# Kernel tuning notes

Hardware: AMD Instinct MI355X
Metric: run time of the kernel (lower is better)

The kernel has to match this reference:

```python
import jax, jax.numpy as jnp
import numpy as np

B, N, D, H, DK = 4, 2048, 1024, 16, 64  # batch, seq, model_dim, heads, key_dim (= value_dim)
NEG = -1e9


def setup_inputs() -> dict:
    key = jax.random.key(0)
    ks = jax.random.split(key, 5)
    X = jax.random.normal(ks[0], (B, N, D), dtype=jnp.float32)
    # causal additive mask [N, N]; module slices mask[:N, :M] and adds to logits
    mask = jnp.where(jnp.tril(jnp.ones((N, N), dtype=bool)), 0.0, NEG).astype(jnp.float32)
    s = 1.0 / np.sqrt(D)
    Wq = jax.random.normal(ks[1], (D, H * DK), dtype=jnp.float32) * s
    Wk = jax.random.normal(ks[2], (D, H * DK), dtype=jnp.float32) * s
    Wv = jax.random.normal(ks[3], (D, H * DK), dtype=jnp.float32) * s
    Wo = jax.random.normal(ks[4], (H * DK, D), dtype=jnp.float32) * s
    return {"X": X, "mask": mask, "Wq": Wq, "Wk": Wk, "Wv": Wv, "Wo": Wo}


def reference(X, mask, Wq, Wk, Wv, Wo):
    # Linear projections (bias=False), then split heads: [B,N,H,DK] -> [B,H,N,DK]
    Q = (X @ Wq).reshape(B, N, H, DK).transpose(0, 2, 1, 3)
    K = (X @ Wk).reshape(B, N, H, DK).transpose(0, 2, 1, 3)
    V = (X @ Wv).reshape(B, N, H, DK).transpose(0, 2, 1, 3)
    # full [B,H,N,N] attention logits (module materializes it explicitly)
    att = jnp.einsum('bhnd,bhmd->bhnm', Q, K) / jnp.sqrt(jnp.float32(DK))
    # dropout is in eval mode here -> identity; then additive mask[:N,:M]
    att = att + mask[:N, :N]
    prob = jax.nn.softmax(att, axis=-1)
    values = jnp.einsum('bhnm,bhmd->bhnd', prob, V)
    values_cat = values.transpose(0, 2, 1, 3).reshape(B, N, H * DK)
    return values_cat @ Wo
```

## Files before the change

### kernel.cpp

```cpp
#include <hip/hip_runtime.h>

typedef __fp16   f2  __attribute__((ext_vector_type(2)));
typedef _Float16 h4  __attribute__((ext_vector_type(4)));
typedef _Float16 v8h __attribute__((ext_vector_type(8)));
typedef float    v4f __attribute__((ext_vector_type(4)));
struct f2x2 { f2 lo, hi; };

#if __has_builtin(__builtin_amdgcn_exp2f)
#define FEXP2(x) __builtin_amdgcn_exp2f(x)
#else
#define FEXP2(x) exp2f(x)
#endif

constexpr int Bn = 4, Nn = 2048, Dn = 1024, Hn = 16, DKn = 64, Mn = 8192;

__device__ __forceinline__ void load_lds16(const _Float16* g, _Float16* l) {
    __builtin_amdgcn_global_load_lds(
        (const __attribute__((address_space(1))) void*)g,
        (__attribute__((address_space(3))) void*)l, 16, 0, 0);
}

__global__ __launch_bounds__(256) void cast_f16(const float* __restrict__ x,
                                                _Float16* __restrict__ y) {
    const int i = blockIdx.x * 256 + threadIdx.x;
    const float4 v = ((const float4*)x)[i];
    h4 o; o[0] = (_Float16)v.x; o[1] = (_Float16)v.y;
    o[2] = (_Float16)v.z; o[3] = (_Float16)v.w;
    ((h4*)y)[i] = o;
}

__global__ __launch_bounds__(256) void castW4(const float* __restrict__ Wq,
                                              const float* __restrict__ Wk,
                                              const float* __restrict__ Wv,
                                              const float* __restrict__ Wo,
                                              _Float16* __restrict__ Wqkv,
                                              _Float16* __restrict__ Wto) {
    __shared__ float tile[32][33];
    const int which = blockIdx.x >> 10, bid = blockIdx.x & 1023;
    const float* W = which == 0 ? Wq : which == 1 ? Wk : which == 2 ? Wv : Wo;
    _Float16* Dst = which < 3 ? (Wqkv + ((size_t)which << 20)) : Wto;
    const int bx = bid & 31, by = bid >> 5;
    const int t = threadIdx.x;
    const int r = t >> 3, c4 = (t & 7) * 4;
    const float4 v = *(const float4*)&W[(size_t)(by * 32 + r) * Dn + bx * 32 + c4];
    tile[r][c4 + 0] = v.x; tile[r][c4 + 1] = v.y;
    tile[r][c4 + 2] = v.z; tile[r][c4 + 3] = v.w;
    __syncthreads();
    h4 o;
    o[0] = (_Float16)tile[c4 + 0][r];
    o[1] = (_Float16)tile[c4 + 1][r];
    o[2] = (_Float16)tile[c4 + 2][r];
    o[3] = (_Float16)tile[c4 + 3][r];
    *(h4*)&Dst[(size_t)(bx * 32 + r) * Dn + by * 32 + c4] = o;
}

#define GEMM_KLOOP64(Abase, Bbase)                                                  \
    v4f acc[4][4];                                                                  \
    _Pragma("unroll") for (int i = 0; i < 4; ++i)                                   \
        _Pragma("unroll") for (int j = 0; j < 4; ++j) acc[i][j] = v4f{0,0,0,0};     \
    for (int k0 = 0; k0 < Dn; k0 += 64) {                                           \
        __syncthreads();                                                            \
        _Pragma("unroll") for (int jj = 0; jj < 4; ++jj) {                          \
            const int ci = jj * 256 + w * 64 + lane;                                \
            const int rs = ci >> 3, cs = ci & 7;                                    \
            const int gc = (cs ^ (rs & 7)) * 8;                                     \
            load_lds16(Abase + (size_t)rs * Dn + k0 + gc, &As[(jj*256 + w*64) * 8]);\
            load_lds16(Bbase + (size_t)rs * Dn + k0 + gc, &Bs[(jj*256 + w*64) * 8]);\
        }                                                                           \
        __syncthreads();                                                            \
        _Pragma("unroll") for (int ks2 = 0; ks2 < 2; ++ks2) {                       \
            v8h a[4], b[4];                                                         \
            _Pragma("unroll") for (int i = 0; i < 4; ++i) {                         \
                const int ar = wm*64 + i*16 + l16;                                  \
                a[i] = *(const v8h*)&As[ar * 64 + (((ks2*4 + quad) ^ (ar & 7)) * 8)];\
            }                                                                       \
            _Pragma("unroll") for (int j = 0; j < 4; ++j) {                         \
                const int br = wn*64 + j*16 + l16;                                  \
                b[j] = *(const v8h*)&Bs[br * 64 + (((ks2*4 + quad) ^ (br & 7)) * 8)];\
            }                                                                       \
            _Pragma("unroll") for (int i = 0; i < 4; ++i)                           \
                _Pragma("unroll") for (int j = 0; j < 4; ++j)                       \
                    acc[i][j] = __builtin_amdgcn_mfma_f32_16x16x32_f16(a[i], b[j],  \
                                                                   acc[i][j],0,0,0);\
        }                                                                           \
    }

__global__ __launch_bounds__(256) void gemmqkv(const _Float16* __restrict__ A,
                                               const _Float16* __restrict__ Wt,
                                               _Float16* __restrict__ Qo,
                                               _Float16* __restrict__ Ko,
                                               _Float16* __restrict__ Vo)
{
    __shared__ __align__(16) _Float16 As[128 * 64];
    __shared__ __align__(16) _Float16 Bs[128 * 64];
    const int t = threadIdx.x, lane = t & 63, w = t >> 6;
    const int quad = lane >> 4, l16 = lane & 15;
    const int wm = w >> 1, wn = w & 1;
    const int bx = blockIdx.x % 24, by = blockIdx.x / 24;
    const int m0 = by * 128, n0 = bx * 128;
    const _Float16* Abase = A + (size_t)m0 * Dn;
    const _Float16* Bbase = Wt + (size_t)n0 * Dn;

    GEMM_KLOOP64(Abase, Bbase)

    const int sec = n0 >> 10;
    if (sec < 2) {
        _Float16* C = sec ? Ko : Qo;
        const float scale = sec ? 1.0f : 0.125f * 1.44269504f;
#pragma unroll
        for (int i = 0; i < 4; ++i) {
            const int mbase = m0 + wm * 64 + i * 16 + quad * 4;
#pragma unroll
            for (int j = 0; j < 4; ++j) {
                const int nl = (n0 + wn * 64 + j * 16 + l16) & 1023;
                const int h = nl >> 6, dk = nl & 63;
#pragma unroll
                for (int r = 0; r < 4; ++r) {
                    const int m = mbase + r, b = m >> 11, nr = m & (Nn - 1);
                    C[((size_t)(b * Hn + h) * Nn + nr) * DKn + dk] = (_Float16)(acc[i][j][r] * scale);
                }
            }
        }
    } else {
#pragma unroll
        for (int i = 0; i < 4; ++i) {
            const int mbase = m0 + wm * 64 + i * 16 + quad * 4;
            const int b = mbase >> 11, nr = mbase & (Nn - 1);
#pragma unroll
            for (int j = 0; j < 4; ++j) {
                const int nl = (n0 + wn * 64 + j * 16 + l16) & 1023;
                const int h = nl >> 6, dk = nl & 63;
                h4 o; o[0] = (_Float16)acc[i][j][0]; o[1] = (_Float16)acc[i][j][1];
                o[2] = (_Float16)acc[i][j][2]; o[3] = (_Float16)acc[i][j][3];
                *(h4*)&Vo[((size_t)(b * Hn + h) * DKn + dk) * Nn + nr] = o;
            }
        }
    }
}

__global__ __launch_bounds__(256) void gemmo(const _Float16* __restrict__ A,
                                             const _Float16* __restrict__ Wt,
                                             float* __restrict__ C)
{
    __shared__ __align__(16) _Float16 As[128 * 64];
    __shared__ __align__(16) _Float16 Bs[128 * 64];
    const int t = threadIdx.x, lane = t & 63, w = t >> 6;
    const int quad = lane >> 4, l16 = lane & 15;
    const int wm = w >> 1, wn = w & 1;
    const int bx = blockIdx.x & 7, by = blockIdx.x >> 3;
    const int m0 = by * 128, n0 = bx * 128;
    const _Float16* Abase = A + (size_t)m0 * Dn;
    const _Float16* Bbase = Wt + (size_t)n0 * Dn;

    GEMM_KLOOP64(Abase, Bbase)

#pragma unroll
    for (int i = 0; i < 4; ++i) {
        const int mbase = m0 + wm * 64 + i * 16 + quad * 4;
#pragma unroll
        for (int j = 0; j < 4; ++j) {
            const int n = n0 + wn * 64 + j * 16 + l16;
#pragma unroll
            for (int r = 0; r < 4; ++r)
                C[(size_t)(mbase + r) * Dn + n] = acc[i][j][r];
        }
    }
}

__global__ __launch_bounds__(256) void flashv5(const _Float16* __restrict__ Q,
                                               const _Float16* __restrict__ K,
                                               const _Float16* __restrict__ Vt,
                                               _Float16* __restrict__ O)
{
    __shared__ __align__(16) _Float16 KS[64 * 64];
    __shared__ __align__(16) _Float16 VS[64 * 64];
    __shared__ __align__(16) _Float16 Ps[4][32 * 64];

    const int t = threadIdx.x;
    const int lane = t & 63, w = t >> 6;
    const int quad = lane >> 4, l16 = lane & 15;
    const int bh = blockIdx.x & 63;
    const int qtile = 15 - (blockIdx.x >> 6);
    const int b = bh >> 4, h = bh & 15;
    const int qb = qtile * 128 + w * 32;

    const _Float16* Qg = Q  + (size_t)bh * Nn * DKn;
    const _Float16* Kg = K  + (size_t)bh * Nn * DKn;
    const _Float16* Vg = Vt + (size_t)bh * DKn * Nn;

    auto stage = [&](int kt) {
        const int k0 = kt * 64;
#pragma unroll
        for (int jj = 0; jj < 2; ++jj) {
            const int ci = jj * 256 + w * 64 + lane;
            const int r = ci >> 3, c = ci & 7;
            const int gc = (c ^ (r & 7)) * 8;
            load_lds16(Kg + (size_t)(k0 + r) * DKn + gc, &KS[(jj * 256 + w * 64) * 8]);
            load_lds16(Vg + (size_t)r * Nn + k0 + gc,    &VS[(jj * 256 + w * 64) * 8]);
        }
    };
#define SWZ(arr, r, c) (*(const v8h*)&(arr)[(r) * 64 + (((c) ^ ((r) & 7)) * 8)])

    v8h qf[2][2];
#pragma unroll
    for (int qq = 0; qq < 2; ++qq)
#pragma unroll
        for (int ks = 0; ks < 2; ++ks)
            qf[qq][ks] = *(const v8h*)&Qg[(size_t)(qb + qq * 16 + l16) * DKn + ks * 32 + quad * 8];

    v8h ones;
#pragma unroll
    for (int i = 0; i < 8; ++i) ones[i] = (_Float16)1.0f;

    v4f o[2][4];
#pragma unroll
    for (int mq = 0; mq < 2; ++mq)
#pragma unroll
        for (int nt = 0; nt < 4; ++nt) o[mq][nt] = v4f{0.f, 0.f, 0.f, 0.f};
    v4f ol[2] = {v4f{0.f, 0.f, 0.f, 0.f}, v4f{0.f, 0.f, 0.f, 0.f}};

    const int NKT  = 2 * qtile + 2;
    const int diag = 2 * qtile + (w >> 1);

    for (int kt = 0; kt < NKT; ++kt) {
        stage(kt);
        __syncthreads();
        if (kt <= diag) {
            const int k0 = kt * 64;
            auto ptile = [&](bool domask) {
#pragma unroll
                for (int kk = 0; kk < 4; ++kk) {
                    v4f s0 = v4f{0.f, 0.f, 0.f, 0.f}, s1 = v4f{0.f, 0.f, 0.f, 0.f};
#pragma unroll
                    for (int ks = 0; ks < 2; ++ks) {
                        const v8h ak = SWZ(KS, kk * 16 + l16, ks * 4 + quad);
                        s0 = __builtin_amdgcn_mfma_f32_16x16x32_f16(ak, qf[0][ks], s0, 0, 0, 0);
                        s1 = __builtin_amdgcn_mfma_f32_16x16x32_f16(ak, qf[1][ks], s1, 0, 0, 0);
                    }
                    const int key0 = k0 + kk * 16 + quad * 4;
#pragma unroll
                    for (int qq = 0; qq < 2; ++qq) {
                        const v4f sv = qq ? s1 : s0;
                        const int q = qb + qq * 16 + l16;
                        float p[4];
#pragma unroll
                        for (int r = 0; r < 4; ++r) {
                            float x = sv[r];
                            if (domask) x = (key0 + r > q) ? -1e9f : x;
                            p[r] = FEXP2(x);
                        }
                        f2x2 pkr;
                        pkr.lo = __builtin_amdgcn_cvt_pkrtz(p[0], p[1]);
                        pkr.hi = __builtin_amdgcn_cvt_pkrtz(p[2], p[3]);
                        const h4 pk = __builtin_bit_cast(h4, pkr);
                        const int prow = qq * 16 + l16;
                        const int pch  = kk * 2 + (quad >> 1);
                        *(h4*)&Ps[w][prow * 64 + ((pch ^ (prow & 7)) * 8 + (quad & 1) * 4)] = pk;
                    }
                }
#pragma unroll
                for (int ks = 0; ks < 2; ++ks)
#pragma unroll
                    for (int mq = 0; mq < 2; ++mq) {
                        const int arow = mq * 16 + l16;
                        const int ach  = ks * 4 + quad;
                        const v8h a = *(const v8h*)&Ps[w][arow * 64 + ((ach ^ (arow & 7)) * 8)];
#pragma unroll
                        for (int nt = 0; nt < 4; ++nt) {
                            const v8h bvv = SWZ(VS, nt * 16 + l16, ks * 4 + quad);
                            o[mq][nt] = __builtin_amdgcn_mfma_f32_16x16x32_f16(a, bvv, o[mq][nt], 0, 0, 0);
                        }
                        ol[mq] = __builtin_amdgcn_mfma_f32_16x16x32_f16(a, ones, ol[mq], 0, 0, 0);
                    }
            };
            if (kt == diag) ptile(true); else ptile(false);
        }
        __syncthreads();
    }
#undef SWZ

    _Float16* Op = O + (size_t)b * Nn * Dn + h * DKn;
#pragma unroll
    for (int mq = 0; mq < 2; ++mq)
#pragma unroll
        for (int r = 0; r < 4; ++r) {
            const float li = 1.0f / ol[mq][r];
            const int qrow = qb + mq * 16 + quad * 4 + r;
#pragma unroll
            for (int nt = 0; nt < 4; ++nt)
                Op[(size_t)qrow * Dn + nt * 16 + l16] = (_Float16)(o[mq][nt][r] * li);
        }
}

extern "C" void kernel_launch(void* const* d_in, const int* in_sizes, int n_in,
                              void* d_out, int out_size, void* d_ws, size_t ws_size,
                              hipStream_t stream)
{
    const float* X  = (const float*)d_in[0];
    const float* Wq = (const float*)d_in[2];
    const float* Wk = (const float*)d_in[3];
    const float* Wv = (const float*)d_in[4];
    const float* Wo = (const float*)d_in[5];

    char* ws = (char*)d_ws;
    _Float16* Xh   = (_Float16*)ws;
    _Float16* Wqkv = (_Float16*)(ws + (16u << 20));
    _Float16* Wto  = Wqkv + (3u << 20);
    _Float16* Qh   = Wto + (1u << 20);
    _Float16* Kh   = Qh + (size_t)Mn * Dn;
    _Float16* Vth  = Kh + (size_t)Mn * Dn;
    _Float16* Ah   = Vth + (size_t)Mn * Dn;

    cast_f16<<<(Mn * Dn / 4) / 256, 256, 0, stream>>>(X, Xh);
    castW4<<<4096, 256, 0, stream>>>(Wq, Wk, Wv, Wo, Wqkv, Wto);
    gemmqkv<<<64 * 24, 256, 0, stream>>>(Xh, Wqkv, Qh, Kh, Vth);
    flashv5<<<1024, 256, 0, stream>>>(Qh, Kh, Vth, Ah);
    gemmo<<<512, 256, 0, stream>>>(Ah, Wto, (float*)d_out);
}
```

Measured before the change: 263.8 us.

## Pipeline projection GEMMs with multi-buffered LDS and larger 256x128 tiles

```diff
diff --git a/kernel.cpp b/kernel.cpp
--- a/kernel.cpp
+++ b/kernel.cpp
@@ -54,115 +54,146 @@
     *(h4*)&Dst[(size_t)(bx * 32 + r) * Dn + by * 32 + c4] = o;
 }
 
-#define GEMM_KLOOP64(Abase, Bbase)                                                  \
-    v4f acc[4][4];                                                                  \
-    _Pragma("unroll") for (int i = 0; i < 4; ++i)                                   \
-        _Pragma("unroll") for (int j = 0; j < 4; ++j) acc[i][j] = v4f{0,0,0,0};     \
-    for (int k0 = 0; k0 < Dn; k0 += 64) {                                           \
-        __syncthreads();                                                            \
-        _Pragma("unroll") for (int jj = 0; jj < 4; ++jj) {                          \
-            const int ci = jj * 256 + w * 64 + lane;                                \
-            const int rs = ci >> 3, cs = ci & 7;                                    \
-            const int gc = (cs ^ (rs & 7)) * 8;                                     \
-            load_lds16(Abase + (size_t)rs * Dn + k0 + gc, &As[(jj*256 + w*64) * 8]);\
-            load_lds16(Bbase + (size_t)rs * Dn + k0 + gc, &Bs[(jj*256 + w*64) * 8]);\
-        }                                                                           \
-        __syncthreads();                                                            \
-        _Pragma("unroll") for (int ks2 = 0; ks2 < 2; ++ks2) {                       \
-            v8h a[4], b[4];                                                         \
-            _Pragma("unroll") for (int i = 0; i < 4; ++i) {                         \
-                const int ar = wm*64 + i*16 + l16;                                  \
-                a[i] = *(const v8h*)&As[ar * 64 + (((ks2*4 + quad) ^ (ar & 7)) * 8)];\
-            }                                                                       \
-            _Pragma("unroll") for (int j = 0; j < 4; ++j) {                         \
-                const int br = wn*64 + j*16 + l16;                                  \
-                b[j] = *(const v8h*)&Bs[br * 64 + (((ks2*4 + quad) ^ (br & 7)) * 8)];\
-            }                                                                       \
-            _Pragma("unroll") for (int i = 0; i < 4; ++i)                           \
-                _Pragma("unroll") for (int j = 0; j < 4; ++j)                       \
-                    acc[i][j] = __builtin_amdgcn_mfma_f32_16x16x32_f16(a[i], b[j],  \
-                                                                   acc[i][j],0,0,0);\
-        }                                                                           \
-    }
-
-__global__ __launch_bounds__(256) void gemmqkv(const _Float16* __restrict__ A,
+#define MFMA16(A, B, C) __builtin_amdgcn_mfma_f32_16x16x32_f16((A), (B), (C), 0, 0, 0)
+
+#define GEMM_PIPE_SETUP()                                                        \
+    __shared__ __align__(16) _Float16 As[2 * 2 * 8192];                          \
+    __shared__ __align__(16) _Float16 Bs[2 * 2 * 4096];                          \
+    const int t = threadIdx.x, lane = t & 63, w = t >> 6;                        \
+    const int quad = lane >> 4, l16 = lane & 15;                                 \
+    const int wm = w & 3, wn = w >> 2;                                           \
+            \
+    const int rA = t >> 2;                                                       \
+    const int gc = ((t & 3) ^ (rA & 3)) * 8;        \
+    const _Float16* pA0 = Abase + (size_t)rA * Dn + gc;                          \
+    const _Float16* pA1 = pA0 + (size_t)128 * Dn; \
+    const _Float16* pB0 = Bbase + (size_t)rA * Dn + gc;                          \
+    _Float16* lA0 = As + w * 512;                                                \
+    _Float16* lA1 = As + 4096 + w * 512;                                         \
+    _Float16* lB0 = Bs + w * 512;                                                \
+    auto stage = [&](int ts, int sh) {                                           \
+        const int reg = (ts & 1) * 2 + sh;                                       \
+        const int ko  = ts * 64 + sh * 32;                                       \
+        load_lds16(pA0 + ko, lA0 + reg * 8192);                                  \
+        load_lds16(pA1 + ko, lA1 + reg * 8192);                                  \
+        load_lds16(pB0 + ko, lB0 + reg * 4096);                                  \
+    };                                                                           \
+        \
+    const int swz  = (quad ^ (l16 & 3)) * 8;                                     \
+    const int aoff = (wm * 64 + l16) * 32 + swz;                                 \
+    const int boff = (wn * 64 + l16) * 32 + swz;                                 \
+    v4f acc[4][4];                                                               \
+    _Pragma("unroll") for (int i = 0; i < 4; ++i)                                \
+        _Pragma("unroll") for (int j = 0; j < 4; ++j) acc[i][j] = v4f{0, 0, 0, 0};\
+    stage(0, 0); stage(0, 1); stage(1, 0);            \
+    asm volatile("s_waitcnt vmcnt(6)" ::: "memory");                             \
+    __builtin_amdgcn_s_barrier();
+
+#define GPHASE(BUF, KH, TS, SH, DOST, VM) do {                                   \
+    const _Float16* Ab_ = As + ((BUF) * 2 + (KH)) * 8192 + aoff;                 \
+    const _Float16* Bb_ = Bs + ((BUF) * 2 + (KH)) * 4096 + boff;                 \
+    v8h a0 = *(const v8h*)(Ab_ +    0), a1 = *(const v8h*)(Ab_ +  512);          \
+    v8h a2 = *(const v8h*)(Ab_ + 1024), a3 = *(const v8h*)(Ab_ + 1536);          \
+    v8h b0 = *(const v8h*)(Bb_ +    0), b1 = *(const v8h*)(Bb_ +  512);          \
+    v8h b2 = *(const v8h*)(Bb_ + 1024), b3 = *(const v8h*)(Bb_ + 1536);          \
+    if (DOST) stage((TS), (SH));                                                 \
+    __builtin_amdgcn_s_barrier();                                                \
+    __builtin_amdgcn_s_setprio(1);                                               \
+    acc[0][0] = MFMA16(a0, b0, acc[0][0]); acc[0][1] = MFMA16(a0, b1, acc[0][1]);\
+    acc[0][2] = MFMA16(a0, b2, acc[0][2]); acc[0][3] = MFMA16(a0, b3, acc[0][3]);\
+    acc[1][0] = MFMA16(a1, b0, acc[1][0]); acc[1][1] = MFMA16(a1, b1, acc[1][1]);\
+    acc[1][2] = MFMA16(a1, b2, acc[1][2]); acc[1][3] = MFMA16(a1, b3, acc[1][3]);\
+    acc[2][0] = MFMA16(a2, b0, acc[2][0]); acc[2][1] = MFMA16(a2, b1, acc[2][1]);\
+    acc[2][2] = MFMA16(a2, b2, acc[2][2]); acc[2][3] = MFMA16(a2, b3, acc[2][3]);\
+    acc[3][0] = MFMA16(a3, b0, acc[3][0]); acc[3][1] = MFMA16(a3, b1, acc[3][1]);\
+    acc[3][2] = MFMA16(a3, b2, acc[3][2]); acc[3][3] = MFMA16(a3, b3, acc[3][3]);\
+    __builtin_amdgcn_s_setprio(0);                                               \
+    asm volatile("s_waitcnt " VM ::: "memory");                                  \
+    __builtin_amdgcn_s_barrier();                                                \
+} while (0)
+
+#define GEMM_PIPE_KLOOP()                                                        \
+    for (int tt = 0; tt < 14; tt += 2) {                                         \
+        GPHASE(0, 0, tt + 1, 1, true, "vmcnt(6)");                               \
+        GPHASE(0, 1, tt + 2, 0, true, "vmcnt(6)");                               \
+        GPHASE(1, 0, tt + 2, 1, true, "vmcnt(6)");                               \
+        GPHASE(1, 1, tt + 3, 0, true, "vmcnt(6)");                               \
+    }                                                                            \
+    GPHASE(0, 0, 15, 1, true,  "vmcnt(6)");       \
+    GPHASE(0, 1, 0, 0, false, "vmcnt(3)");                             \
+    GPHASE(1, 0, 0, 0, false, "vmcnt(0)");                             \
+    GPHASE(1, 1, 0, 0, false, "vmcnt(0)");
+
+__global__ __launch_bounds__(512) void gemmqkv(const _Float16* __restrict__ A,
                                                const _Float16* __restrict__ Wt,
                                                _Float16* __restrict__ Qo,
                                                _Float16* __restrict__ Ko,
                                                _Float16* __restrict__ Vo)
 {
-    __shared__ __align__(16) _Float16 As[128 * 64];
-    __shared__ __align__(16) _Float16 Bs[128 * 64];
-    const int t = threadIdx.x, lane = t & 63, w = t >> 6;
-    const int quad = lane >> 4, l16 = lane & 15;
-    const int wm = w >> 1, wn = w & 1;
     const int bx = blockIdx.x % 24, by = blockIdx.x / 24;
-    const int m0 = by * 128, n0 = bx * 128;
+    const int m0 = by * 256, n0 = bx * 128;
     const _Float16* Abase = A + (size_t)m0 * Dn;
     const _Float16* Bbase = Wt + (size_t)n0 * Dn;
 
-    GEMM_KLOOP64(Abase, Bbase)
+    GEMM_PIPE_SETUP()
+    GEMM_PIPE_KLOOP()
 
     const int sec = n0 >> 10;
     if (sec < 2) {
         _Float16* C = sec ? Ko : Qo;
         const float scale = sec ? 1.0f : 0.125f * 1.44269504f;
 #pragma unroll
-        for (int i = 0; i < 4; ++i) {
-            const int mbase = m0 + wm * 64 + i * 16 + quad * 4;
-#pragma unroll
-            for (int j = 0; j < 4; ++j) {
-                const int nl = (n0 + wn * 64 + j * 16 + l16) & 1023;
+        for (int mf = 0; mf < 4; ++mf) {
+            const int mbase = m0 + wm * 64 + mf * 16 + quad * 4;
+#pragma unroll
+            for (int nf = 0; nf < 4; ++nf) {
+                const int nl = (n0 + wn * 64 + nf * 16 + l16) & 1023;
                 const int h = nl >> 6, dk = nl & 63;
 #pragma unroll
                 for (int r = 0; r < 4; ++r) {
                     const int m = mbase + r, b = m >> 11, nr = m & (Nn - 1);
-                    C[((size_t)(b * Hn + h) * Nn + nr) * DKn + dk] = (_Float16)(acc[i][j][r] * scale);
+                    C[((size_t)(b * Hn + h) * Nn + nr) * DKn + dk] = (_Float16)(acc[mf][nf][r] * scale);
                 }
             }
         }
     } else {
 #pragma unroll
-        for (int i = 0; i < 4; ++i) {
-            const int mbase = m0 + wm * 64 + i * 16 + quad * 4;
+        for (int mf = 0; mf < 4; ++mf) {
+            const int mbase = m0 + wm * 64 + mf * 16 + quad * 4;
             const int b = mbase >> 11, nr = mbase & (Nn - 1);
 #pragma unroll
-            for (int j = 0; j < 4; ++j) {
-                const int nl = (n0 + wn * 64 + j * 16 + l16) & 1023;
+            for (int nf = 0; nf < 4; ++nf) {
+                const int nl = (n0 + wn * 64 + nf * 16 + l16) & 1023;
                 const int h = nl >> 6, dk = nl & 63;
-                h4 o; o[0] = (_Float16)acc[i][j][0]; o[1] = (_Float16)acc[i][j][1];
-                o[2] = (_Float16)acc[i][j][2]; o[3] = (_Float16)acc[i][j][3];
+                h4 o; o[0] = (_Float16)acc[mf][nf][0]; o[1] = (_Float16)acc[mf][nf][1];
+                o[2] = (_Float16)acc[mf][nf][2]; o[3] = (_Float16)acc[mf][nf][3];
                 *(h4*)&Vo[((size_t)(b * Hn + h) * DKn + dk) * Nn + nr] = o;
             }
         }
     }
 }
 
-__global__ __launch_bounds__(256) void gemmo(const _Float16* __restrict__ A,
+__global__ __launch_bounds__(512) void gemmo(const _Float16* __restrict__ A,
                                              const _Float16* __restrict__ Wt,
                                              float* __restrict__ C)
 {
-    __shared__ __align__(16) _Float16 As[128 * 64];
-    __shared__ __align__(16) _Float16 Bs[128 * 64];
-    const int t = threadIdx.x, lane = t & 63, w = t >> 6;
-    const int quad = lane >> 4, l16 = lane & 15;
-    const int wm = w >> 1, wn = w & 1;
     const int bx = blockIdx.x & 7, by = blockIdx.x >> 3;
-    const int m0 = by * 128, n0 = bx * 128;
+    const int m0 = by * 256, n0 = bx * 128;
     const _Float16* Abase = A + (size_t)m0 * Dn;
     const _Float16* Bbase = Wt + (size_t)n0 * Dn;
 
-    GEMM_KLOOP64(Abase, Bbase)
-
-#pragma unroll
-    for (int i = 0; i < 4; ++i) {
-        const int mbase = m0 + wm * 64 + i * 16 + quad * 4;
-#pragma unroll
-        for (int j = 0; j < 4; ++j) {
-            const int n = n0 + wn * 64 + j * 16 + l16;
+    GEMM_PIPE_SETUP()
+    GEMM_PIPE_KLOOP()
+
+#pragma unroll
+    for (int mf = 0; mf < 4; ++mf) {
+        const int mbase = m0 + wm * 64 + mf * 16 + quad * 4;
+#pragma unroll
+        for (int nf = 0; nf < 4; ++nf) {
+            const int n = n0 + wn * 64 + nf * 16 + l16;
 #pragma unroll
             for (int r = 0; r < 4; ++r)
-                C[(size_t)(mbase + r) * Dn + n] = acc[i][j][r];
+                C[(size_t)(mbase + r) * Dn + n] = acc[mf][nf][r];
         }
     }
 }
@@ -313,7 +344,7 @@
 
     cast_f16<<<(Mn * Dn / 4) / 256, 256, 0, stream>>>(X, Xh);
     castW4<<<4096, 256, 0, stream>>>(Wq, Wk, Wv, Wo, Wqkv, Wto);
-    gemmqkv<<<64 * 24, 256, 0, stream>>>(Xh, Wqkv, Qh, Kh, Vth);
+    gemmqkv<<<768, 512, 0, stream>>>(Xh, Wqkv, Qh, Kh, Vth);
     flashv5<<<1024, 256, 0, stream>>>(Qh, Kh, Vth, Ah);
-    gemmo<<<512, 256, 0, stream>>>(Ah, Wto, (float*)d_out);
-}
+    gemmo<<<256, 512, 0, stream>>>(Ah, Wto, (float*)d_out);
+}
```

Measured after the change: 261.6 us. No clear change (-0.9%).
